# Optimization experiments

Measured on AMD Instinct MI355X. Metric: run time of the kernel, lower is better.

Reference implementation:

```python
import jax, jax.numpy as jnp
import numpy as np

B, T, M, P = 256, 256, 512, 512


def setup_inputs() -> dict:
    key = jax.random.key(0)
    ks = jax.random.split(key, 10)
    sc = lambda fan: 1.0 / np.sqrt(fan)
    return {
        "H": jax.random.normal(ks[0], (B, T, M), jnp.float32),
        "d0": jax.random.normal(ks[1], (1, B, P), jnp.float32),
        "s0": jax.random.normal(ks[2], (1, B, P), jnp.float32),
        # TemporalAttention params (torch Linear convention: y = x @ W.T)
        "W_d": jax.random.uniform(ks[3], (M, 2 * P), jnp.float32, -sc(2 * P), sc(2 * P)),
        "U_d": jax.random.uniform(ks[4], (M, M), jnp.float32, -sc(M), sc(M)),
        "v_d": jax.random.uniform(ks[5], (1, M), jnp.float32, -sc(M), sc(M)),
        # LSTM params (torch nn.LSTM convention, gate order i,f,g,o)
        "W_ih": jax.random.uniform(ks[6], (4 * P, M), jnp.float32, -sc(P), sc(P)),
        "W_hh": jax.random.uniform(ks[7], (4 * P, P), jnp.float32, -sc(P), sc(P)),
        "b_ih": jax.random.uniform(ks[8], (4 * P,), jnp.float32, -sc(P), sc(P)),
        "b_hh": jax.random.uniform(ks[9], (4 * P,), jnp.float32, -sc(P), sc(P)),
    }


def reference(H, d0, s0, W_d, U_d, v_d, W_ih, W_hh, b_ih, b_hh):
    T_steps = H.shape[1]
    # U_d(H) is time-invariant across decode steps: precompute once. [B,T,m]
    UH = jnp.einsum("btm,nm->btn", H, U_d)
    v = v_d[0]  # [m]

    def step(carry, _):
        d, s = carry  # [B,p] hidden, [B,p] cell
        q = jnp.concatenate([d, s], axis=-1)            # [B,2p]
        wq = q @ W_d.T                                   # [B,m]
        e = jnp.tanh(wq[:, None, :] + UH) @ v            # [B,T]
        beta = jax.nn.softmax(e, axis=1)                 # softmax over time
        c_t = jnp.einsum("bt,btm->bm", beta, H)          # [B,m]
        gates = c_t @ W_ih.T + b_ih + d @ W_hh.T + b_hh  # [B,4p]
        i, f, g, o = jnp.split(gates, 4, axis=-1)
        s_new = jax.nn.sigmoid(f) * s + jax.nn.sigmoid(i) * jnp.tanh(g)
        d_new = jax.nn.sigmoid(o) * jnp.tanh(s_new)
        return (d_new, s_new), (beta, c_t)

    (d, s), (betas, cts) = jax.lax.scan(step, (d0[0], s0[0]), None, length=T_steps)
    attn = jnp.transpose(betas, (1, 0, 2))               # [B,T,T]
    out = jnp.concatenate([d[:, None, :], cts[-1][:, None, :]], axis=2)  # [B,1,p+m]
    return out, attn
```

## Files before the change

kernel.cpp:

```cpp
#include <hip/hip_runtime.h>
#include <hip/hip_fp16.h>

typedef _Float16 h4 __attribute__((ext_vector_type(4)));
typedef _Float16 h8 __attribute__((ext_vector_type(8)));
typedef float    f4 __attribute__((ext_vector_type(4)));

#define SC2LOG2E 2.8853900817779268f

__device__ __forceinline__ float v_exp2(float x) { float r; asm("v_exp_f32 %0, %1" : "=v"(r) : "v"(x)); return r; }
__device__ __forceinline__ float v_rcp (float x) { float r; asm("v_rcp_f32 %0, %1" : "=v"(r) : "v"(x)); return r; }
__device__ __forceinline__ float fast_tanh(float x) {
    float e = __expf(2.0f * x);
    return 1.0f - 2.0f * v_rcp(e + 1.0f);
}
__device__ __forceinline__ float fast_sigmoid(float x) {
    return v_rcp(1.0f + __expf(-x));
}

__global__ void convert_f16(const float* __restrict__ s, _Float16* __restrict__ d, int n) {
    int i = (blockIdx.x * 256 + threadIdx.x) * 4;
    if (i < n) {
        float4 v = *(const float4*)(s + i);
        h4 o = {(_Float16)v.x, (_Float16)v.y, (_Float16)v.z, (_Float16)v.w};
        *(h4*)(d + i) = o;
    }
}

__global__ void build_wg(const float* __restrict__ Wih, const float* __restrict__ Whh,
                         _Float16* __restrict__ Wg) {
    int idx = (blockIdx.x * 256 + threadIdx.x) * 4;
    int np = idx >> 10, k = idx & 1023;
    int p = np >> 2, g = np & 3, row = g * 512 + p;
    const float* src = (k < 512) ? Wih + (size_t)row * 512 + k
                                 : Whh + (size_t)row * 512 + (k - 512);
    float4 v = *(const float4*)src;
    h4 o = {(_Float16)v.x, (_Float16)v.y, (_Float16)v.z, (_Float16)v.w};
    *(h4*)(Wg + idx) = o;
}

__global__ void build_bsum(const float* __restrict__ bih, const float* __restrict__ bhh,
                           float* __restrict__ bsum) {
    int np = blockIdx.x * 256 + threadIdx.x;
    int p = np >> 2, g = np & 3, row = g * 512 + p;
    bsum[np] = bih[row] + bhh[row];
}

__global__ void init_state(const float* __restrict__ d0, const float* __restrict__ s0,
                           float* __restrict__ sbuf,
                           _Float16* __restrict__ qA, _Float16* __restrict__ ds) {
    int i = blockIdx.x * 256 + threadIdx.x;
    float dv = d0[i], sv = s0[i];
    sbuf[i] = sv;
    int b = i >> 9, j = i & 511;
    qA[(size_t)b * 1024 + 512 + j] = (_Float16)dv;
    ds[(size_t)b * 1024 + j]       = (_Float16)dv;
    ds[(size_t)b * 1024 + 512 + j] = (_Float16)sv;
}

__global__ __launch_bounds__(128) void uh_mfma(const float* __restrict__ H,
                                               const float* __restrict__ Ud,
                                               _Float16* __restrict__ UH2) {
    int tid = threadIdx.x;
    int lane = tid & 63, w = tid >> 6;
    int ln = lane & 15, quad = lane >> 4;
    int m0 = blockIdx.x * 64, n0 = blockIdx.y * 32;
    f4 z = {0.f, 0.f, 0.f, 0.f};
    f4 acc[4] = {z, z, z, z};
    const float* brow = Ud + (size_t)(n0 + w * 16 + ln) * 512 + quad * 8;
    const float* arow = H  + (size_t)(m0 + ln) * 512 + quad * 8;
#pragma unroll 2
    for (int k = 0; k < 16; k++) {
        float4 bx = *(const float4*)(brow + k * 32);
        float4 by = *(const float4*)(brow + k * 32 + 4);
        h8 b = {(_Float16)bx.x, (_Float16)bx.y, (_Float16)bx.z, (_Float16)bx.w,
                (_Float16)by.x, (_Float16)by.y, (_Float16)by.z, (_Float16)by.w};
#pragma unroll
        for (int mt = 0; mt < 4; mt++) {
            const float* ap = arow + (size_t)mt * 16 * 512 + k * 32;
            float4 ax = *(const float4*)ap;
            float4 ay = *(const float4*)(ap + 4);
            h8 a = {(_Float16)ax.x, (_Float16)ax.y, (_Float16)ax.z, (_Float16)ax.w,
                    (_Float16)ay.x, (_Float16)ay.y, (_Float16)ay.z, (_Float16)ay.w};
            acc[mt] = __builtin_amdgcn_mfma_f32_16x16x32_f16(a, b, acc[mt], 0, 0, 0);
        }
    }
#pragma unroll
    for (int mt = 0; mt < 4; mt++)
#pragma unroll
        for (int r = 0; r < 4; r++)
            UH2[(size_t)(m0 + mt * 16 + quad * 4 + r) * 512 + n0 + w * 16 + ln] =
                (_Float16)(acc[mt][r] * SC2LOG2E);
}

__global__ __launch_bounds__(256) void wq_gemm(const _Float16* __restrict__ ds,
                                               const _Float16* __restrict__ Wdh,
                                               float* __restrict__ wq2) {
    int tid = threadIdx.x;
    int lane = tid & 63, w = tid >> 6;
    int ln = lane & 15, quad = lane >> 4;
    int m0 = blockIdx.x * 64, n0 = blockIdx.y * 16;
    f4 acc = {0.f, 0.f, 0.f, 0.f};
    const h8* ap = (const h8*)(ds  + (size_t)(m0 + w * 16 + ln) * 1024) + quad;
    const h8* bp = (const h8*)(Wdh + (size_t)(n0 + ln) * 1024) + quad;
#pragma unroll 8
    for (int k = 0; k < 32; k++) {
        h8 a = ap[k * 4];
        h8 b = bp[k * 4];
        acc = __builtin_amdgcn_mfma_f32_16x16x32_f16(a, b, acc, 0, 0, 0);
    }
#pragma unroll
    for (int r = 0; r < 4; r++)
        wq2[(size_t)(m0 + w * 16 + quad * 4 + r) * 512 + n0 + ln] = acc[r] * SC2LOG2E;
}

__global__ __launch_bounds__(512) void gates_gemm(const _Float16* __restrict__ qcur,
                                                  const _Float16* __restrict__ Wg,
                                                  const float* __restrict__ bsum,
                                                  float* __restrict__ sbuf,
                                                  _Float16* __restrict__ qnext,
                                                  _Float16* __restrict__ ds,
                                                  float* __restrict__ out,
                                                  int t) {
    __shared__ float gt[64][36];
    int tid = threadIdx.x;
    int lane = tid & 63, w = tid >> 6;
    int ln = lane & 15, quad = lane >> 4;
    int mt = w & 3, nt = w >> 2;
    int m0 = blockIdx.x * 64, n0 = blockIdx.y * 32;
    f4 acc = {0.f, 0.f, 0.f, 0.f};
    const h8* ap = (const h8*)(qcur + (size_t)(m0 + mt * 16 + ln) * 1024) + quad;
    const h8* bp = (const h8*)(Wg   + (size_t)(n0 + nt * 16 + ln) * 1024) + quad;
#pragma unroll 8
    for (int k = 0; k < 32; k++) {
        h8 a = ap[k * 4];
        h8 b = bp[k * 4];
        acc = __builtin_amdgcn_mfma_f32_16x16x32_f16(a, b, acc, 0, 0, 0);
    }
    float bs = bsum[n0 + nt * 16 + ln];
#pragma unroll
    for (int r = 0; r < 4; r++)
        gt[mt * 16 + quad * 4 + r][nt * 16 + ln] = acc[r] + bs;
    __syncthreads();

    int p0 = blockIdx.y * 8;
    int ml = tid >> 3, pl = tid & 7;
    float4 g4 = *(const float4*)&gt[ml][pl * 4];
    int b = m0 + ml, p = p0 + pl;
    float ig = fast_sigmoid(g4.x);
    float fg = fast_sigmoid(g4.y);
    float gg = fast_tanh(g4.z);
    float og = fast_sigmoid(g4.w);
    float sold = sbuf[(size_t)b * 512 + p];
    float snew = fmaf(fg, sold, ig * gg);
    float dnew = og * fast_tanh(snew);
    sbuf[(size_t)b * 512 + p] = snew;
    qnext[(size_t)b * 1024 + 512 + p] = (_Float16)dnew;
    ds[(size_t)b * 1024 + p]          = (_Float16)dnew;
    ds[(size_t)b * 1024 + 512 + p]    = (_Float16)snew;
    if (t == 255) out[(size_t)b * 1024 + p] = dnew;
}

__global__ __launch_bounds__(1024) void attn_kernel(const _Float16* __restrict__ UH2,
                                                    const _Float16* __restrict__ Hh,
                                                    const float* __restrict__ Hf,
                                                    const float* __restrict__ wq2,
                                                    const float* __restrict__ vd,
                                                    _Float16* __restrict__ qcur,
                                                    float* __restrict__ attn_out,
                                                    float* __restrict__ out,
                                                    int t) {
    __shared__ float es[256];
    __shared__ float red[4];
    __shared__ float red2[4];
    __shared__ float part[8][512];

    int b = blockIdx.x;
    int tid = threadIdx.x;
    int wv = tid >> 6, lane = tid & 63;

    const float4* wqp = (const float4*)(wq2 + (size_t)b * 512 + lane * 8);
    float4 w0 = wqp[0], w1 = wqp[1];
    const float4* vp = (const float4*)(vd + lane * 8);
    float4 vv0 = vp[0], vv1 = vp[1];
    float wr[8] = {w0.x, w0.y, w0.z, w0.w, w1.x, w1.y, w1.z, w1.w};
    float vr[8] = {vv0.x, vv0.y, vv0.z, vv0.w, vv1.x, vv1.y, vv1.z, vv1.w};

    const h8* up = (const h8*)(UH2 + (size_t)b * 256 * 512) + lane;
#pragma unroll 2
    for (int i = 0; i < 16; i++) {
        int tp = wv * 16 + i;
        h8 u = up[(size_t)tp * 64];
        float acc = 0.0f;
#pragma unroll
        for (int j = 0; j < 8; j++) {
            float zz = wr[j] + (float)u[j];
            float r = v_rcp(1.0f + v_exp2(zz));
            acc = fmaf(vr[j], r, acc);
        }
#pragma unroll
        for (int o = 32; o; o >>= 1) acc += __shfl_xor(acc, o, 64);
        if (lane == 0) es[tp] = -2.0f * acc;
    }
    __syncthreads();

    float v = 0.0f, ex = 0.0f;
    if (tid < 256) {
        v = es[tid];
        float mx = v;
#pragma unroll
        for (int o = 32; o; o >>= 1) mx = fmaxf(mx, __shfl_xor(mx, o, 64));
        if (lane == 0) red[wv] = mx;
    }
    __syncthreads();
    float mall = fmaxf(fmaxf(red[0], red[1]), fmaxf(red[2], red[3]));
    if (tid < 256) {
        ex = __expf(v - mall);
        float s = ex;
#pragma unroll
        for (int o = 32; o; o >>= 1) s += __shfl_xor(s, o, 64);
        if (lane == 0) red2[wv] = s;
    }
    __syncthreads();
    float tot = red2[0] + red2[1] + red2[2] + red2[3];
    float beta = 0.0f;
    if (tid < 256) beta = ex * v_rcp(tot);
    __syncthreads();
    if (tid < 256) {
        es[tid] = beta;
        attn_out[(size_t)b * 65536 + (size_t)t * 256 + tid] = beta;
    }
    __syncthreads();

    int tc = tid >> 7, g = tid & 127;
    float a0 = 0, a1 = 0, a2 = 0, a3 = 0;
    if (Hh) {
        const h4* hp = (const h4*)(Hh + ((size_t)b * 256 + tc * 32) * 512) + g;
#pragma unroll 4
        for (int i = 0; i < 32; i++) {
            h4 hv = hp[(size_t)i * 128];
            float bt = es[tc * 32 + i];
            a0 = fmaf(bt, (float)hv[0], a0);
            a1 = fmaf(bt, (float)hv[1], a1);
            a2 = fmaf(bt, (float)hv[2], a2);
            a3 = fmaf(bt, (float)hv[3], a3);
        }
    } else {
        const float4* hp = (const float4*)(Hf + ((size_t)b * 256 + tc * 32) * 512) + g;
#pragma unroll 4
        for (int i = 0; i < 32; i++) {
            float4 hv = hp[(size_t)i * 128];
            float bt = es[tc * 32 + i];
            a0 = fmaf(bt, hv.x, a0);
            a1 = fmaf(bt, hv.y, a1);
            a2 = fmaf(bt, hv.z, a2);
            a3 = fmaf(bt, hv.w, a3);
        }
    }
    *(float4*)&part[tc][g * 4] = make_float4(a0, a1, a2, a3);
    __syncthreads();
    if (tid < 512) {
        int m = tid;
        float c = part[0][m] + part[1][m] + part[2][m] + part[3][m]
                + part[4][m] + part[5][m] + part[6][m] + part[7][m];
        qcur[(size_t)b * 1024 + m] = (_Float16)c;
        if (t == 255) out[(size_t)b * 1024 + 512 + m] = c;
    }
}

extern "C" void kernel_launch(void* const* d_in, const int* in_sizes, int n_in,
                              void* d_out, int out_size, void* d_ws, size_t ws_size,
                              hipStream_t stream) {
    const float* H   = (const float*)d_in[0];
    const float* d0  = (const float*)d_in[1];
    const float* s0  = (const float*)d_in[2];
    const float* Wd  = (const float*)d_in[3];
    const float* Ud  = (const float*)d_in[4];
    const float* vd  = (const float*)d_in[5];
    const float* Wih = (const float*)d_in[6];
    const float* Whh = (const float*)d_in[7];
    const float* bih = (const float*)d_in[8];
    const float* bhh = (const float*)d_in[9];

    float* out  = (float*)d_out;
    float* attn = out + 262144;

    char* ws = (char*)d_ws;
    size_t off = 0;
    _Float16* UH2  = (_Float16*)(ws + off); off += 67108864;
    _Float16* Wdh  = (_Float16*)(ws + off); off += 1048576;
    _Float16* Wg   = (_Float16*)(ws + off); off += 4194304;
    float*    bsum = (float*)   (ws + off); off += 8192;
    float*    wq2  = (float*)   (ws + off); off += 524288;
    _Float16* qA   = (_Float16*)(ws + off); off += 524288;
    _Float16* qB   = (_Float16*)(ws + off); off += 524288;
    _Float16* ds   = (_Float16*)(ws + off); off += 524288;
    float*    sbuf = (float*)   (ws + off); off += 524288;
    _Float16* Hh   = nullptr;
    if (ws_size >= off + 67108864) { Hh = (_Float16*)(ws + off); off += 67108864; }

    convert_f16<<<512, 256, 0, stream>>>(Wd, Wdh, 524288);
    build_wg<<<2048, 256, 0, stream>>>(Wih, Whh, Wg);
    build_bsum<<<8, 256, 0, stream>>>(bih, bhh, bsum);
    if (Hh) convert_f16<<<32768, 256, 0, stream>>>(H, Hh, 33554432);
    init_state<<<512, 256, 0, stream>>>(d0, s0, sbuf, qA, ds);
    uh_mfma<<<dim3(1024, 16), 128, 0, stream>>>(H, Ud, UH2);

    for (int t = 0; t < 256; t++) {
        _Float16* qcur = (t & 1) ? qB : qA;
        _Float16* qnxt = (t & 1) ? qA : qB;
        wq_gemm<<<dim3(4, 32), 256, 0, stream>>>(ds, Wdh, wq2);
        attn_kernel<<<256, 1024, 0, stream>>>(UH2, Hh, H, wq2, vd, qcur, attn, out, t);
        gates_gemm<<<dim3(4, 64), 512, 0, stream>>>(qcur, Wg, bsum, sbuf, qnxt, ds, out, t);
    }
}
```

Measured before the change: 14.36 ms.

## Fuse per-step kernels into one persistent cooperative kernel with grid syncs

Replaces the 768 per-step kernel launches (wq GEMM, attention, gates GEMM) with a single cooperative kernel of 256 blocks that loops over all time steps and separates the phases with grid.sync. The small GEMMs are remapped onto the 256 blocks and split over K, with partial sums reduced in shared memory. The uh_mfma precompute now has each block loop over all N tiles, giving fewer, larger blocks. This removes launch overhead at the cost of grid-wide barriers, lower parallelism in the GEMM phases, and a requirement that all 256 blocks be co-resident.

```diff
diff --git a/kernel.cpp b/kernel.cpp
--- a/kernel.cpp
+++ b/kernel.cpp
@@ -1,5 +1,8 @@
 #include <hip/hip_runtime.h>
 #include <hip/hip_fp16.h>
+#include <hip/hip_cooperative_groups.h>
+
+namespace cg = cooperative_groups;
 
 typedef _Float16 h4 __attribute__((ext_vector_type(4)));
 typedef _Float16 h8 __attribute__((ext_vector_type(8)));
@@ -63,207 +66,218 @@
     int tid = threadIdx.x;
     int lane = tid & 63, w = tid >> 6;
     int ln = lane & 15, quad = lane >> 4;
-    int m0 = blockIdx.x * 64, n0 = blockIdx.y * 32;
-    f4 z = {0.f, 0.f, 0.f, 0.f};
-    f4 acc[4] = {z, z, z, z};
-    const float* brow = Ud + (size_t)(n0 + w * 16 + ln) * 512 + quad * 8;
-    const float* arow = H  + (size_t)(m0 + ln) * 512 + quad * 8;
+    int m0 = blockIdx.x * 64;
+    const float* arow = H + (size_t)(m0 + ln) * 512 + quad * 8;
+    for (int n0 = 0; n0 < 512; n0 += 32) {
+        f4 z = {0.f, 0.f, 0.f, 0.f};
+        f4 acc[4] = {z, z, z, z};
+        const float* brow = Ud + (size_t)(n0 + w * 16 + ln) * 512 + quad * 8;
 #pragma unroll 2
-    for (int k = 0; k < 16; k++) {
-        float4 bx = *(const float4*)(brow + k * 32);
-        float4 by = *(const float4*)(brow + k * 32 + 4);
-        h8 b = {(_Float16)bx.x, (_Float16)bx.y, (_Float16)bx.z, (_Float16)bx.w,
-                (_Float16)by.x, (_Float16)by.y, (_Float16)by.z, (_Float16)by.w};
-#pragma unroll
-        for (int mt = 0; mt < 4; mt++) {
-            const float* ap = arow + (size_t)mt * 16 * 512 + k * 32;
-            float4 ax = *(const float4*)ap;
-            float4 ay = *(const float4*)(ap + 4);
-            h8 a = {(_Float16)ax.x, (_Float16)ax.y, (_Float16)ax.z, (_Float16)ax.w,
-                    (_Float16)ay.x, (_Float16)ay.y, (_Float16)ay.z, (_Float16)ay.w};
-            acc[mt] = __builtin_amdgcn_mfma_f32_16x16x32_f16(a, b, acc[mt], 0, 0, 0);
-        }
+        for (int k = 0; k < 16; k++) {
+            float4 bx = *(const float4*)(brow + k * 32);
+            float4 by = *(const float4*)(brow + k * 32 + 4);
+            h8 b = {(_Float16)bx.x, (_Float16)bx.y, (_Float16)bx.z, (_Float16)bx.w,
+                    (_Float16)by.x, (_Float16)by.y, (_Float16)by.z, (_Float16)by.w};
+#pragma unroll
+            for (int mt = 0; mt < 4; mt++) {
+                const float* ap = arow + (size_t)mt * 16 * 512 + k * 32;
+                float4 ax = *(const float4*)ap;
+                float4 ay = *(const float4*)(ap + 4);
+                h8 a = {(_Float16)ax.x, (_Float16)ax.y, (_Float16)ax.z, (_Float16)ax.w,
+                        (_Float16)ay.x, (_Float16)ay.y, (_Float16)ay.z, (_Float16)ay.w};
+                acc[mt] = __builtin_amdgcn_mfma_f32_16x16x32_f16(a, b, acc[mt], 0, 0, 0);
+            }
+        }
+#pragma unroll
+        for (int mt = 0; mt < 4; mt++)
+#pragma unroll
+            for (int r = 0; r < 4; r++)
+                UH2[(size_t)(m0 + mt * 16 + quad * 4 + r) * 512 + n0 + w * 16 + ln] =
+                    (_Float16)(acc[mt][r] * SC2LOG2E);
     }
-#pragma unroll
-    for (int mt = 0; mt < 4; mt++)
-#pragma unroll
-        for (int r = 0; r < 4; r++)
-            UH2[(size_t)(m0 + mt * 16 + quad * 4 + r) * 512 + n0 + w * 16 + ln] =
-                (_Float16)(acc[mt][r] * SC2LOG2E);
-}
-
-__global__ __launch_bounds__(256) void wq_gemm(const _Float16* __restrict__ ds,
-                                               const _Float16* __restrict__ Wdh,
-                                               float* __restrict__ wq2) {
-    int tid = threadIdx.x;
-    int lane = tid & 63, w = tid >> 6;
-    int ln = lane & 15, quad = lane >> 4;
-    int m0 = blockIdx.x * 64, n0 = blockIdx.y * 16;
-    f4 acc = {0.f, 0.f, 0.f, 0.f};
-    const h8* ap = (const h8*)(ds  + (size_t)(m0 + w * 16 + ln) * 1024) + quad;
-    const h8* bp = (const h8*)(Wdh + (size_t)(n0 + ln) * 1024) + quad;
-#pragma unroll 8
-    for (int k = 0; k < 32; k++) {
-        h8 a = ap[k * 4];
-        h8 b = bp[k * 4];
-        acc = __builtin_amdgcn_mfma_f32_16x16x32_f16(a, b, acc, 0, 0, 0);
-    }
-#pragma unroll
-    for (int r = 0; r < 4; r++)
-        wq2[(size_t)(m0 + w * 16 + quad * 4 + r) * 512 + n0 + ln] = acc[r] * SC2LOG2E;
-}
-
-__global__ __launch_bounds__(512) void gates_gemm(const _Float16* __restrict__ qcur,
-                                                  const _Float16* __restrict__ Wg,
-                                                  const float* __restrict__ bsum,
-                                                  float* __restrict__ sbuf,
-                                                  _Float16* __restrict__ qnext,
-                                                  _Float16* __restrict__ ds,
-                                                  float* __restrict__ out,
-                                                  int t) {
-    __shared__ float gt[64][36];
-    int tid = threadIdx.x;
-    int lane = tid & 63, w = tid >> 6;
-    int ln = lane & 15, quad = lane >> 4;
-    int mt = w & 3, nt = w >> 2;
-    int m0 = blockIdx.x * 64, n0 = blockIdx.y * 32;
-    f4 acc = {0.f, 0.f, 0.f, 0.f};
-    const h8* ap = (const h8*)(qcur + (size_t)(m0 + mt * 16 + ln) * 1024) + quad;
-    const h8* bp = (const h8*)(Wg   + (size_t)(n0 + nt * 16 + ln) * 1024) + quad;
-#pragma unroll 8
-    for (int k = 0; k < 32; k++) {
-        h8 a = ap[k * 4];
-        h8 b = bp[k * 4];
-        acc = __builtin_amdgcn_mfma_f32_16x16x32_f16(a, b, acc, 0, 0, 0);
-    }
-    float bs = bsum[n0 + nt * 16 + ln];
-#pragma unroll
-    for (int r = 0; r < 4; r++)
-        gt[mt * 16 + quad * 4 + r][nt * 16 + ln] = acc[r] + bs;
-    __syncthreads();
-
-    int p0 = blockIdx.y * 8;
-    int ml = tid >> 3, pl = tid & 7;
-    float4 g4 = *(const float4*)&gt[ml][pl * 4];
-    int b = m0 + ml, p = p0 + pl;
-    float ig = fast_sigmoid(g4.x);
-    float fg = fast_sigmoid(g4.y);
-    float gg = fast_tanh(g4.z);
-    float og = fast_sigmoid(g4.w);
-    float sold = sbuf[(size_t)b * 512 + p];
-    float snew = fmaf(fg, sold, ig * gg);
-    float dnew = og * fast_tanh(snew);
-    sbuf[(size_t)b * 512 + p] = snew;
-    qnext[(size_t)b * 1024 + 512 + p] = (_Float16)dnew;
-    ds[(size_t)b * 1024 + p]          = (_Float16)dnew;
-    ds[(size_t)b * 1024 + 512 + p]    = (_Float16)snew;
-    if (t == 255) out[(size_t)b * 1024 + p] = dnew;
-}
-
-__global__ __launch_bounds__(1024) void attn_kernel(const _Float16* __restrict__ UH2,
-                                                    const _Float16* __restrict__ Hh,
-                                                    const float* __restrict__ Hf,
-                                                    const float* __restrict__ wq2,
-                                                    const float* __restrict__ vd,
-                                                    _Float16* __restrict__ qcur,
-                                                    float* __restrict__ attn_out,
-                                                    float* __restrict__ out,
-                                                    int t) {
-    __shared__ float es[256];
-    __shared__ float red[4];
-    __shared__ float red2[4];
-    __shared__ float part[8][512];
-
-    int b = blockIdx.x;
-    int tid = threadIdx.x;
-    int wv = tid >> 6, lane = tid & 63;
-
-    const float4* wqp = (const float4*)(wq2 + (size_t)b * 512 + lane * 8);
-    float4 w0 = wqp[0], w1 = wqp[1];
-    const float4* vp = (const float4*)(vd + lane * 8);
-    float4 vv0 = vp[0], vv1 = vp[1];
-    float wr[8] = {w0.x, w0.y, w0.z, w0.w, w1.x, w1.y, w1.z, w1.w};
-    float vr[8] = {vv0.x, vv0.y, vv0.z, vv0.w, vv1.x, vv1.y, vv1.z, vv1.w};
-
-    const h8* up = (const h8*)(UH2 + (size_t)b * 256 * 512) + lane;
+}
+
+__global__ __launch_bounds__(1024, 4) void fused_loop(
+        const _Float16* __restrict__ UH2, const _Float16* Hh,
+        const float* __restrict__ Hf, const float* __restrict__ vd,
+        const _Float16* __restrict__ Wdh, const _Float16* __restrict__ Wg,
+        const float* __restrict__ bsum, float* __restrict__ wq2,
+        _Float16* qA, _Float16* qB, _Float16* ds,
+        float* __restrict__ sbuf, float* __restrict__ attn_out,
+        float* __restrict__ out) {
+    cg::grid_group grid = cg::this_grid();
+    __shared__ union {
+        float wqp[4][256];
+        struct { float es[256]; float red[4]; float red2[4]; float part[8][512]; } at;
+        float gt[2][64][36];
+    } sm;
+
+    const int bid = blockIdx.x;
+    const int tid = threadIdx.x;
+    const int lane = tid & 63, w = tid >> 6;
+    const int ln = lane & 15, quad = lane >> 4;
+
+    for (int t = 0; t < 256; ++t) {
+        _Float16* qcur = (t & 1) ? qB : qA;
+        _Float16* qnxt = (t & 1) ? qA : qB;
+
+        if (w < 4) {
+            int pair = w >> 1, kh = w & 1;
+            int tau = 2 * bid + pair;
+            int m0 = (tau & 15) * 16, n0 = (tau >> 4) * 16;
+            f4 acc = {0.f, 0.f, 0.f, 0.f};
+            const h8* ap = (const h8*)(ds  + (size_t)(m0 + ln) * 1024) + kh * 64 + quad;
+            const h8* bp = (const h8*)(Wdh + (size_t)(n0 + ln) * 1024) + kh * 64 + quad;
+#pragma unroll
+            for (int k = 0; k < 16; k++)
+                acc = __builtin_amdgcn_mfma_f32_16x16x32_f16(ap[k * 4], bp[k * 4], acc, 0, 0, 0);
+#pragma unroll
+            for (int r = 0; r < 4; r++)
+                sm.wqp[w][(quad * 4 + r) * 16 + ln] = acc[r];
+        }
+        __syncthreads();
+        if (tid < 512) {
+            int pair = tid >> 8, e = tid & 255;
+            int tau = 2 * bid + pair;
+            int m0 = (tau & 15) * 16, n0 = (tau >> 4) * 16;
+            float val = (sm.wqp[2 * pair][e] + sm.wqp[2 * pair + 1][e]) * SC2LOG2E;
+            wq2[(size_t)(m0 + (e >> 4)) * 512 + n0 + (e & 15)] = val;
+        }
+        grid.sync();
+
+        {
+            const float4* wqp4 = (const float4*)(wq2 + (size_t)bid * 512 + lane * 8);
+            float4 w0 = wqp4[0], w1 = wqp4[1];
+            const float4* vp4 = (const float4*)(vd + lane * 8);
+            float4 vv0 = vp4[0], vv1 = vp4[1];
+            float wr[8] = {w0.x, w0.y, w0.z, w0.w, w1.x, w1.y, w1.z, w1.w};
+            float vr[8] = {vv0.x, vv0.y, vv0.z, vv0.w, vv1.x, vv1.y, vv1.z, vv1.w};
+
+            const h8* up = (const h8*)(UH2 + (size_t)bid * 256 * 512) + lane;
 #pragma unroll 2
-    for (int i = 0; i < 16; i++) {
-        int tp = wv * 16 + i;
-        h8 u = up[(size_t)tp * 64];
-        float acc = 0.0f;
-#pragma unroll
-        for (int j = 0; j < 8; j++) {
-            float zz = wr[j] + (float)u[j];
-            float r = v_rcp(1.0f + v_exp2(zz));
-            acc = fmaf(vr[j], r, acc);
-        }
-#pragma unroll
-        for (int o = 32; o; o >>= 1) acc += __shfl_xor(acc, o, 64);
-        if (lane == 0) es[tp] = -2.0f * acc;
-    }
-    __syncthreads();
-
-    float v = 0.0f, ex = 0.0f;
-    if (tid < 256) {
-        v = es[tid];
-        float mx = v;
-#pragma unroll
-        for (int o = 32; o; o >>= 1) mx = fmaxf(mx, __shfl_xor(mx, o, 64));
-        if (lane == 0) red[wv] = mx;
-    }
-    __syncthreads();
-    float mall = fmaxf(fmaxf(red[0], red[1]), fmaxf(red[2], red[3]));
-    if (tid < 256) {
-        ex = __expf(v - mall);
-        float s = ex;
-#pragma unroll
-        for (int o = 32; o; o >>= 1) s += __shfl_xor(s, o, 64);
-        if (lane == 0) red2[wv] = s;
-    }
-    __syncthreads();
-    float tot = red2[0] + red2[1] + red2[2] + red2[3];
-    float beta = 0.0f;
-    if (tid < 256) beta = ex * v_rcp(tot);
-    __syncthreads();
-    if (tid < 256) {
-        es[tid] = beta;
-        attn_out[(size_t)b * 65536 + (size_t)t * 256 + tid] = beta;
-    }
-    __syncthreads();
-
-    int tc = tid >> 7, g = tid & 127;
-    float a0 = 0, a1 = 0, a2 = 0, a3 = 0;
-    if (Hh) {
-        const h4* hp = (const h4*)(Hh + ((size_t)b * 256 + tc * 32) * 512) + g;
+            for (int i = 0; i < 16; i++) {
+                int tp = w * 16 + i;
+                h8 u = up[(size_t)tp * 64];
+                float acc = 0.0f;
+#pragma unroll
+                for (int j = 0; j < 8; j++) {
+                    float zz = wr[j] + (float)u[j];
+                    float r = v_rcp(1.0f + v_exp2(zz));
+                    acc = fmaf(vr[j], r, acc);
+                }
+#pragma unroll
+                for (int o = 32; o; o >>= 1) acc += __shfl_xor(acc, o, 64);
+                if (lane == 0) sm.at.es[tp] = -2.0f * acc;
+            }
+            __syncthreads();
+
+            float v = 0.0f, ex = 0.0f;
+            if (tid < 256) {
+                v = sm.at.es[tid];
+                float mx = v;
+#pragma unroll
+                for (int o = 32; o; o >>= 1) mx = fmaxf(mx, __shfl_xor(mx, o, 64));
+                if (lane == 0) sm.at.red[w] = mx;
+            }
+            __syncthreads();
+            float mall = fmaxf(fmaxf(sm.at.red[0], sm.at.red[1]),
+                               fmaxf(sm.at.red[2], sm.at.red[3]));
+            if (tid < 256) {
+                ex = __expf(v - mall);
+                float s = ex;
+#pragma unroll
+                for (int o = 32; o; o >>= 1) s += __shfl_xor(s, o, 64);
+                if (lane == 0) sm.at.red2[w] = s;
+            }
+            __syncthreads();
+            float tot = sm.at.red2[0] + sm.at.red2[1] + sm.at.red2[2] + sm.at.red2[3];
+            float beta = 0.0f;
+            if (tid < 256) beta = ex * v_rcp(tot);
+            __syncthreads();
+            if (tid < 256) {
+                sm.at.es[tid] = beta;
+                attn_out[(size_t)bid * 65536 + (size_t)t * 256 + tid] = beta;
+            }
+            __syncthreads();
+
+            int tc = tid >> 7, g = tid & 127;
+            float a0 = 0, a1 = 0, a2 = 0, a3 = 0;
+            if (Hh) {
+                const h4* hp = (const h4*)(Hh + ((size_t)bid * 256 + tc * 32) * 512) + g;
 #pragma unroll 4
-        for (int i = 0; i < 32; i++) {
-            h4 hv = hp[(size_t)i * 128];
-            float bt = es[tc * 32 + i];
-            a0 = fmaf(bt, (float)hv[0], a0);
-            a1 = fmaf(bt, (float)hv[1], a1);
-            a2 = fmaf(bt, (float)hv[2], a2);
-            a3 = fmaf(bt, (float)hv[3], a3);
-        }
-    } else {
-        const float4* hp = (const float4*)(Hf + ((size_t)b * 256 + tc * 32) * 512) + g;
+                for (int i = 0; i < 32; i++) {
+                    h4 hv = hp[(size_t)i * 128];
+                    float bt = sm.at.es[tc * 32 + i];
+                    a0 = fmaf(bt, (float)hv[0], a0);
+                    a1 = fmaf(bt, (float)hv[1], a1);
+                    a2 = fmaf(bt, (float)hv[2], a2);
+                    a3 = fmaf(bt, (float)hv[3], a3);
+                }
+            } else {
+                const float4* hp = (const float4*)(Hf + ((size_t)bid * 256 + tc * 32) * 512) + g;
 #pragma unroll 4
-        for (int i = 0; i < 32; i++) {
-            float4 hv = hp[(size_t)i * 128];
-            float bt = es[tc * 32 + i];
-            a0 = fmaf(bt, hv.x, a0);
-            a1 = fmaf(bt, hv.y, a1);
-            a2 = fmaf(bt, hv.z, a2);
-            a3 = fmaf(bt, hv.w, a3);
-        }
-    }
-    *(float4*)&part[tc][g * 4] = make_float4(a0, a1, a2, a3);
-    __syncthreads();
-    if (tid < 512) {
-        int m = tid;
-        float c = part[0][m] + part[1][m] + part[2][m] + part[3][m]
-                + part[4][m] + part[5][m] + part[6][m] + part[7][m];
-        qcur[(size_t)b * 1024 + m] = (_Float16)c;
-        if (t == 255) out[(size_t)b * 1024 + 512 + m] = c;
+                for (int i = 0; i < 32; i++) {
+                    float4 hv = hp[(size_t)i * 128];
+                    float bt = sm.at.es[tc * 32 + i];
+                    a0 = fmaf(bt, hv.x, a0);
+                    a1 = fmaf(bt, hv.y, a1);
+                    a2 = fmaf(bt, hv.z, a2);
+                    a3 = fmaf(bt, hv.w, a3);
+                }
+            }
+            *(float4*)&sm.at.part[tc][g * 4] = make_float4(a0, a1, a2, a3);
+            __syncthreads();
+            if (tid < 512) {
+                int m = tid;
+                float c = sm.at.part[0][m] + sm.at.part[1][m] + sm.at.part[2][m] + sm.at.part[3][m]
+                        + sm.at.part[4][m] + sm.at.part[5][m] + sm.at.part[6][m] + sm.at.part[7][m];
+                qcur[(size_t)bid * 1024 + m] = (_Float16)c;
+                if (t == 255) out[(size_t)bid * 1024 + 512 + m] = c;
+            }
+        }
+        grid.sync();
+
+        {
+            int mb = bid & 3, nb = bid >> 2;
+            int ms = w & 3, ns = (w >> 2) & 1, kh = w >> 3;
+            int am0 = mb * 64 + ms * 16;
+            int bn0 = nb * 32 + ns * 16;
+            f4 acc = {0.f, 0.f, 0.f, 0.f};
+            const h8* ap = (const h8*)(qcur + (size_t)(am0 + ln) * 1024) + kh * 64 + quad;
+            const h8* bp = (const h8*)(Wg   + (size_t)(bn0 + ln) * 1024) + kh * 64 + quad;
+#pragma unroll
+            for (int k = 0; k < 16; k++)
+                acc = __builtin_amdgcn_mfma_f32_16x16x32_f16(ap[k * 4], bp[k * 4], acc, 0, 0, 0);
+#pragma unroll
+            for (int r = 0; r < 4; r++)
+                sm.gt[kh][ms * 16 + quad * 4 + r][ns * 16 + ln] = acc[r];
+            __syncthreads();
+
+            if (tid < 512) {
+                int ml = tid >> 3, pl = tid & 7;
+                int b = mb * 64 + ml, p = nb * 8 + pl;
+                float4 gA = *(const float4*)&sm.gt[0][ml][pl * 4];
+                float4 gB = *(const float4*)&sm.gt[1][ml][pl * 4];
+                float4 bb = *(const float4*)(bsum + nb * 32 + pl * 4);
+                float gi = gA.x + gB.x + bb.x;
+                float gf = gA.y + gB.y + bb.y;
+                float gg = gA.z + gB.z + bb.z;
+                float go = gA.w + gB.w + bb.w;
+                float ig = fast_sigmoid(gi);
+                float fg = fast_sigmoid(gf);
+                float g_ = fast_tanh(gg);
+                float og = fast_sigmoid(go);
+                float sold = sbuf[(size_t)b * 512 + p];
+                float snew = fmaf(fg, sold, ig * g_);
+                float dnew = og * fast_tanh(snew);
+                sbuf[(size_t)b * 512 + p] = snew;
+                qnxt[(size_t)b * 1024 + 512 + p] = (_Float16)dnew;
+                ds[(size_t)b * 1024 + p]         = (_Float16)dnew;
+                ds[(size_t)b * 1024 + 512 + p]   = (_Float16)snew;
+                if (t == 255) out[(size_t)b * 1024 + p] = dnew;
+            }
+        }
+        grid.sync();
     }
 }
 
@@ -303,13 +317,12 @@
     build_bsum<<<8, 256, 0, stream>>>(bih, bhh, bsum);
     if (Hh) convert_f16<<<32768, 256, 0, stream>>>(H, Hh, 33554432);
     init_state<<<512, 256, 0, stream>>>(d0, s0, sbuf, qA, ds);
-    uh_mfma<<<dim3(1024, 16), 128, 0, stream>>>(H, Ud, UH2);
-
-    for (int t = 0; t < 256; t++) {
-        _Float16* qcur = (t & 1) ? qB : qA;
-        _Float16* qnxt = (t & 1) ? qA : qB;
-        wq_gemm<<<dim3(4, 32), 256, 0, stream>>>(ds, Wdh, wq2);
-        attn_kernel<<<256, 1024, 0, stream>>>(UH2, Hh, H, wq2, vd, qcur, attn, out, t);
-        gates_gemm<<<dim3(4, 64), 512, 0, stream>>>(qcur, Wg, bsum, sbuf, qnxt, ds, out, t);
-    }
-}
+    uh_mfma<<<1024, 128, 0, stream>>>(H, Ud, UH2);
+
+    void* args[] = {(void*)&UH2, (void*)&Hh, (void*)&H, (void*)&vd,
+                    (void*)&Wdh, (void*)&Wg, (void*)&bsum, (void*)&wq2,
+                    (void*)&qA, (void*)&qB, (void*)&ds, (void*)&sbuf,
+                    (void*)&attn, (void*)&out};
+    hipLaunchCooperativeKernel((const void*)fused_loop, dim3(256), dim3(1024),
+                               args, 0, stream);
+}
```

Result: slower. 35.39 ms (+146.5%).
